# Kernel tuning notes

Hardware: AMD Instinct MI355X
Metric: run time of the kernel (lower is better)

## Reference

```python
import jax, jax.numpy as jnp
import numpy as np
from jax import lax

H = 512   # hidden_size
R = 4     # read heads
W = 32    # memory word size
N = 64    # memory cells
B = 64    # batch
T = 256   # seq len
IFACE = R * W + 3 * W + 5 * R + 3      # 247
HID_C = H + IFACE                       # 759 controller LSTM hidden
IN_C = H + R * W                        # 640 controller LSTM input
EPS = 1e-6


def setup_inputs() -> dict:
    key = jax.random.key(0)
    ks = jax.random.split(key, 7)
    s = 0.05
    return {
        "x": jax.random.normal(ks[0], (B, T, H), jnp.float32),
        "Wih_e": jax.random.normal(ks[1], (4 * H, H), jnp.float32) * s,
        "Whh_e": jax.random.normal(ks[2], (4 * H, H), jnp.float32) * s,
        "b_e": jnp.zeros((4 * H,), jnp.float32),
        "Wih_c": jax.random.normal(ks[3], (4 * HID_C, IN_C), jnp.float32) * s,
        "Whh_c": jax.random.normal(ks[4], (4 * HID_C, HID_C), jnp.float32) * s,
        "b_c": jnp.zeros((4 * HID_C,), jnp.float32),
    }


def lstm_cell(xt, h, c, Wih, Whh, b):
    g = xt @ Wih.T + h @ Whh.T + b
    i, f, gg, o = jnp.split(g, 4, axis=-1)  # PyTorch gate order i,f,g,o
    c = jax.nn.sigmoid(f) * c + jax.nn.sigmoid(i) * jnp.tanh(gg)
    h = jax.nn.sigmoid(o) * jnp.tanh(c)
    return h, c


def content_weights(M, keys, strengths):
    # M: [B,N,W], keys: [B,K,W], strengths: [B,K] -> softmaxed similarity [B,K,N]
    Mn = M * lax.rsqrt(jnp.sum(M * M, -1, keepdims=True) + EPS)
    kn = keys * lax.rsqrt(jnp.sum(keys * keys, -1, keepdims=True) + EPS)
    sim = jnp.einsum('bkw,bnw->bkn', kn, Mn)
    return jax.nn.softmax(sim * strengths[..., None], axis=-1)


def reference(x, Wih_e, Whh_e, b_e, Wih_c, Whh_c, b_c):
    # ---- encoder LSTM over time ----
    def enc_step(carry, xt):
        h, c = carry
        h, c = lstm_cell(xt, h, c, Wih_e, Whh_e, b_e)
        return (h, c), h

    z = jnp.zeros((B, H), x.dtype)
    _, enc = lax.scan(enc_step, (z, z), x.transpose(1, 0, 2))  # [T,B,H]

    # ---- controller LSTM + DNC memory per timestep ----
    eye = jnp.eye(N, dtype=x.dtype)

    def dnc_step(carry, e_t):
        h, c, M, u, p, L, wr, ww, rv = carry
        x_t = jnp.concatenate([e_t, rv], axis=-1)          # [B, H + R*W]
        h, c = lstm_cell(x_t, h, c, Wih_c, Whh_c, b_c)
        out = h[:, :H]
        xi = h[:, H:]                                       # [B, IFACE]
        o = 0
        read_keys = jnp.tanh(xi[:, :R * W].reshape(B, R, W)); o = R * W
        read_str = jax.nn.softplus(xi[:, o:o + R]); o += R
        write_key = jnp.tanh(xi[:, o:o + W]).reshape(B, 1, W); o += W
        write_str = jax.nn.softplus(xi[:, o:o + 1]); o += 1
        erase = jax.nn.sigmoid(xi[:, o:o + W]); o += W
        write_vec = jnp.tanh(xi[:, o:o + W]); o += W
        free_g = jax.nn.sigmoid(xi[:, o:o + R]); o += R
        alloc_g = jax.nn.sigmoid(xi[:, o:o + 1]); o += 1
        write_g = jax.nn.sigmoid(xi[:, o:o + 1]); o += 1
        read_modes = jax.nn.softmax(xi[:, o:o + 3 * R].reshape(B, R, 3), -1)
        # usage + retention
        psi = jnp.prod(1.0 - free_g[..., None] * wr, axis=1)   # [B,N]
        u = (u + ww - u * ww) * psi
        # allocation weighting via sorted usage
        idx = jnp.argsort(u, axis=-1)
        su = jnp.take_along_axis(u, idx, -1)
        cp = jnp.concatenate([jnp.ones((B, 1), u.dtype), jnp.cumprod(su, -1)[:, :-1]], -1)
        a = jnp.take_along_axis((1.0 - su) * cp, jnp.argsort(idx, -1), -1)
        # write weighting
        cw = content_weights(M, write_key, write_str)[:, 0]    # [B,N]
        ww = write_g * (alloc_g * a + (1.0 - alloc_g) * cw)
        # memory write
        M = M * (1.0 - ww[..., None] * erase[:, None, :]) + ww[..., None] * write_vec[:, None, :]
        # temporal link + precedence
        L = (1.0 - ww[:, :, None] - ww[:, None, :]) * L + ww[:, :, None] * p[:, None, :]
        L = L * (1.0 - eye)
        p = (1.0 - jnp.sum(ww, -1, keepdims=True)) * p + ww
        # read weighting: backward, content, forward modes
        cr = content_weights(M, read_keys, read_str)           # [B,R,N]
        fw = jnp.einsum('bnm,brm->brn', L, wr)
        bw = jnp.einsum('bmn,brm->brn', L, wr)
        wr = read_modes[..., 0:1] * bw + read_modes[..., 1:2] * cr + read_modes[..., 2:3] * fw
        rv = jnp.einsum('brn,bnw->brw', wr, M).reshape(B, R * W)
        return (h, c, M, u, p, L, wr, ww, rv), out

    init = (
        jnp.zeros((B, HID_C), x.dtype), jnp.zeros((B, HID_C), x.dtype),
        jnp.zeros((B, N, W), x.dtype), jnp.zeros((B, N), x.dtype),
        jnp.zeros((B, N), x.dtype), jnp.zeros((B, N, N), x.dtype),
        jnp.zeros((B, R, N), x.dtype), jnp.zeros((B, N), x.dtype),
        jnp.zeros((B, R * W), x.dtype),
    )
    _, outs = lax.scan(dnc_step, init, enc)   # [T,B,H]
    return outs.transpose(1, 0, 2)            # dnc_encoded [B,T,H]
```

## Files before the change

### kernel.cpp

```cpp
#include <hip/hip_runtime.h>
#include <math.h>


#define EPSF 1e-6f

__device__ __forceinline__ float sigmoidf_(float x) { return 1.f / (1.f + expf(-x)); }
__device__ __forceinline__ float softplusf_(float x) {
    return (x > 0.f) ? x + log1pf(expf(-x)) : log1pf(expf(x));
}
__device__ __forceinline__ void stg_coh(float* p, float v) {
    __hip_atomic_store(p, v, __ATOMIC_RELAXED, __HIP_MEMORY_SCOPE_AGENT);
}
__device__ __forceinline__ void st_flag(int* p, int v) {
    __hip_atomic_store(p, v, __ATOMIC_RELAXED, __HIP_MEMORY_SCOPE_AGENT);
}
__device__ __forceinline__ int ld_flag(const int* p) {
    return __hip_atomic_load(p, __ATOMIC_RELAXED, __HIP_MEMORY_SCOPE_AGENT);
}
__device__ __forceinline__ void poll256(const int* f, int lane, int tgt) {
    const int* p = f + lane * 32;
    for (;;) {
        int a = ld_flag(p);
        int b = ld_flag(p + 64 * 32);
        int c = ld_flag(p + 128 * 32);
        int d = ld_flag(p + 192 * 32);
        if (__all(min(min(a, b), min(c, d)) >= tgt)) break;
        __builtin_amdgcn_s_sleep(2);
    }
}
__device__ __forceinline__ void pollg(const int* f, int lane, int tgt) {
    const int* p = f + (64 + lane) * 32;
    for (;;) {
        int a = ld_flag(p);
        int b = ld_flag(p + 64 * 32);
        int c = ld_flag(p + 128 * 32);
        if (__all(min(min(a, b), c) >= tgt)) break;
        __builtin_amdgcn_s_sleep(2);
    }
}
__device__ __forceinline__ void pollx(const int* f, int lane, int tgt) {
    const int* p = f + (192 + (lane < 62 ? lane : 61)) * 32;
    while (!__all(ld_flag(p) >= tgt)) __builtin_amdgcn_s_sleep(2);
}
__device__ __forceinline__ void pollm(const int* f2, int lane, int tgt) {
    while (!__all(ld_flag(f2 + lane * 32) >= tgt)) __builtin_amdgcn_s_sleep(2);
}

__global__ __launch_bounds__(256) void prep_weights(const float* __restrict__ Whh_c,
                                                    const float* __restrict__ Wih_c,
                                                    float* __restrict__ Wcat) {
    int idx = blockIdx.x * 256 + threadIdx.x;
    if (idx < 3036 * 896) {
        int r = idx / 896, j = idx - r * 896;
        float v;
        if (j < 759) v = Whh_c[r * 759 + j];
        else if (j < 768) v = 0.f;
        else v = Wih_c[r * 640 + 512 + (j - 768)];
        Wcat[idx] = v;
    }
}

__global__ __launch_bounds__(256, 2) void proj_gemm(const float* __restrict__ A,
                                                    const float* __restrict__ W,
                                                    const float* __restrict__ bias,
                                                    float* __restrict__ OUT, int Ncols,
                                                    int wstride, int arow_base, int arow_stride_t,
                                                    int arow_stride_b, int arowlen, int Mrows) {
    __shared__ float As[16 * 68];
    __shared__ float Ws[16 * 68];
    const int tid = threadIdx.x;
    const int ntile = blockIdx.x, mtile = blockIdx.y;
    const int tx = tid & 15, ty = tid >> 4;
    const int lr = tid >> 2;
    const int lk = (tid & 3) * 4;
    const size_t arow =
        (size_t)arow_base + (size_t)mtile * arow_stride_t + (size_t)lr * arow_stride_b;
    const float* aptr = A + arow * arowlen + lk;
    const int wn = ntile * 64 + lr;
    const bool wok = (wn < Ncols);
    const float* wptr = W + (size_t)(wok ? wn : 0) * wstride + lk;
    float acc[4][4] = {};
    for (int kt = 0; kt < 512; kt += 16) {
        float4 av = *(const float4*)(aptr + kt);
        float4 w4l = *(const float4*)(wptr + kt);
        if (!wok) w4l = make_float4(0.f, 0.f, 0.f, 0.f);
        __syncthreads();
        As[(lk + 0) * 68 + lr] = av.x;
        As[(lk + 1) * 68 + lr] = av.y;
        As[(lk + 2) * 68 + lr] = av.z;
        As[(lk + 3) * 68 + lr] = av.w;
        Ws[(lk + 0) * 68 + lr] = w4l.x;
        Ws[(lk + 1) * 68 + lr] = w4l.y;
        Ws[(lk + 2) * 68 + lr] = w4l.z;
        Ws[(lk + 3) * 68 + lr] = w4l.w;
        __syncthreads();
#pragma unroll
        for (int k = 0; k < 16; ++k) {
            float4 a4 = *(const float4*)&As[k * 68 + ty * 4];
            float4 w4 = *(const float4*)&Ws[k * 68 + tx * 4];
            acc[0][0] = fmaf(a4.x, w4.x, acc[0][0]);
            acc[0][1] = fmaf(a4.x, w4.y, acc[0][1]);
            acc[0][2] = fmaf(a4.x, w4.z, acc[0][2]);
            acc[0][3] = fmaf(a4.x, w4.w, acc[0][3]);
            acc[1][0] = fmaf(a4.y, w4.x, acc[1][0]);
            acc[1][1] = fmaf(a4.y, w4.y, acc[1][1]);
            acc[1][2] = fmaf(a4.y, w4.z, acc[1][2]);
            acc[1][3] = fmaf(a4.y, w4.w, acc[1][3]);
            acc[2][0] = fmaf(a4.z, w4.x, acc[2][0]);
            acc[2][1] = fmaf(a4.z, w4.y, acc[2][1]);
            acc[2][2] = fmaf(a4.z, w4.z, acc[2][2]);
            acc[2][3] = fmaf(a4.z, w4.w, acc[2][3]);
            acc[3][0] = fmaf(a4.w, w4.x, acc[3][0]);
            acc[3][1] = fmaf(a4.w, w4.y, acc[3][1]);
            acc[3][2] = fmaf(a4.w, w4.z, acc[3][2]);
            acc[3][3] = fmaf(a4.w, w4.w, acc[3][3]);
        }
    }
    const int col0 = ntile * 64 + tx * 4;
    const int row0 = mtile * 64 + ty * 4;
#pragma unroll
    for (int j = 0; j < 4; ++j) {
        int col = col0 + j;
        if (col < Ncols) {
            float bv = bias[col];
            float4 st = make_float4(acc[0][j] + bv, acc[1][j] + bv, acc[2][j] + bv,
                                    acc[3][j] + bv);
            *(float4*)&OUT[(size_t)col * Mrows + row0] = st;
        }
    }
}

__global__ __launch_bounds__(256) void enc_emit(const float* __restrict__ HSE,
                                                float* __restrict__ ENC, int t0) {
    const int tl = blockIdx.x, bgrp = blockIdx.y;
    const int c4 = threadIdx.x & 127, b = bgrp * 2 + (threadIdx.x >> 7);
    float4 v = *(const float4*)&HSE[(size_t)tl * 32768 + c4 * 256 + b * 4];
    *(float4*)&ENC[((size_t)(t0 + tl) * 64 + b) * 512 + c4 * 4] = v;
}
__global__ __launch_bounds__(256) void out_emit(const float* __restrict__ HS,
                                                float* __restrict__ OUT, int t0) {
    const int tl = blockIdx.x, bgrp = blockIdx.y;
    const int c4 = threadIdx.x & 127, b = bgrp * 2 + (threadIdx.x >> 7);
    float4 v = *(const float4*)&HS[(size_t)tl * 57344 + c4 * 256 + b * 4];
    *(float4*)&OUT[(size_t)b * 131072 + (size_t)(t0 + tl) * 512 + c4 * 4] = v;
}

__global__ __launch_bounds__(512, 1) void enc_seq(const float* __restrict__ Whh,
                                                  const float* __restrict__ XPT,
                                                  float* __restrict__ HSE,
                                                  float* __restrict__ CE, int M, int TC,
                                                  int* flags) {
    __shared__ float part[8 * 4 * 64];
    const int tid = threadIdx.x;
    const int bk = blockIdx.x;
    const int lane = tid & 63;
    const int wv = __builtin_amdgcn_readfirstlane(tid >> 6);
    const int q = wv & 3, cidx = wv >> 2;
    const int cell = bk + 256 * cidx;
    const float* __restrict__ w0 = Whh + ((size_t)(0 * 512 + cell)) * 512 + q * 128;
    const float* __restrict__ w1 = Whh + ((size_t)(1 * 512 + cell)) * 512 + q * 128;
    const float* __restrict__ w2 = Whh + ((size_t)(2 * 512 + cell)) * 512 + q * 128;
    const float* __restrict__ w3 = Whh + ((size_t)(3 * 512 + cell)) * 512 + q * 128;
    float c_reg = 0.f;
    if (q == 0) c_reg = CE[cell * 64 + lane];
    for (int tl = 0; tl < TC; ++tl) {
        const float* rslot = HSE + (size_t)((tl + TC - 1) % TC) * 32768;
        float* wslot = HSE + (size_t)tl * 32768;
        float x0 = 0.f, x1 = 0.f, x2 = 0.f, x3 = 0.f;
        if (q == 0) {
            const int m = tl * 64 + lane;
            x0 = XPT[(size_t)(0 * 512 + cell) * M + m];
            x1 = XPT[(size_t)(1 * 512 + cell) * M + m];
            x2 = XPT[(size_t)(2 * 512 + cell) * M + m];
            x3 = XPT[(size_t)(3 * 512 + cell) * M + m];
        }
        float a0 = 0.f, a1 = 0.f, a2 = 0.f, a3 = 0.f;
        {
            const float4* __restrict__ hx = (const float4*)rslot + q * 32 * 64;
#pragma unroll 8
            for (int i = 0; i < 32; ++i) {
                float4 hv = hx[i * 64 + lane];
                float4 q0 = *(const float4*)&w0[i * 4];
                float4 q1 = *(const float4*)&w1[i * 4];
                float4 q2 = *(const float4*)&w2[i * 4];
                float4 q3 = *(const float4*)&w3[i * 4];
                a0 = fmaf(hv.x, q0.x, a0); a0 = fmaf(hv.y, q0.y, a0);
                a0 = fmaf(hv.z, q0.z, a0); a0 = fmaf(hv.w, q0.w, a0);
                a1 = fmaf(hv.x, q1.x, a1); a1 = fmaf(hv.y, q1.y, a1);
                a1 = fmaf(hv.z, q1.z, a1); a1 = fmaf(hv.w, q1.w, a1);
                a2 = fmaf(hv.x, q2.x, a2); a2 = fmaf(hv.y, q2.y, a2);
                a2 = fmaf(hv.z, q2.z, a2); a2 = fmaf(hv.w, q2.w, a2);
                a3 = fmaf(hv.x, q3.x, a3); a3 = fmaf(hv.y, q3.y, a3);
                a3 = fmaf(hv.z, q3.z, a3); a3 = fmaf(hv.w, q3.w, a3);
            }
        }
        part[(wv * 4 + 0) * 64 + lane] = a0;
        part[(wv * 4 + 1) * 64 + lane] = a1;
        part[(wv * 4 + 2) * 64 + lane] = a2;
        part[(wv * 4 + 3) * 64 + lane] = a3;
        __syncthreads();
        if (q == 0) {
            float g4[4];
#pragma unroll
            for (int g = 0; g < 4; ++g) {
                g4[g] = part[((cidx * 4 + 0) * 4 + g) * 64 + lane] +
                        part[((cidx * 4 + 1) * 4 + g) * 64 + lane] +
                        part[((cidx * 4 + 2) * 4 + g) * 64 + lane] +
                        part[((cidx * 4 + 3) * 4 + g) * 64 + lane];
            }
            float cc = sigmoidf_(g4[1] + x1) * c_reg + sigmoidf_(g4[0] + x0) * tanhf(g4[2] + x2);
            float hh = sigmoidf_(g4[3] + x3) * tanhf(cc);
            c_reg = cc;
            stg_coh(&wslot[(cell >> 2) * 256 + lane * 4 + (cell & 3)], hh);
        }
        __syncthreads();
        if (tid == 0) st_flag(flags + bk * 32, tl + 1);
        if (tl + 1 < TC) {
            if (wv == 0) poll256(flags, lane, tl + 1);
            __syncthreads();
        }
    }
    if (q == 0) CE[cell * 64 + lane] = c_reg;
}

__global__ __launch_bounds__(1024, 1) void dnc_seq(
    const float* __restrict__ Wcat, const float* __restrict__ CPT, float* __restrict__ HS,
    float* __restrict__ CC, float* __restrict__ Mg, float* __restrict__ Ug,
    float* __restrict__ Pg, float* __restrict__ WWg, float* __restrict__ Lg,
    float* __restrict__ WRg, int M, int TC, int* flags) {
    __shared__ float part[16 * 4 * 64];
    __shared__ float M_l[64 * 33];
    __shared__ float L_l[64 * 65];
    __shared__ float act[256];
    __shared__ float wr_l[256];
    __shared__ float u_l[64], p_l[64], ww_l[64], sM2[64], srt_l[64], asrt_l[64];
    __shared__ float modes_l[12], kss_l[4], scal[4];

    const int tid = threadIdx.x;
    const int bk = blockIdx.x;
    const int lane = tid & 63;
    const int wv = __builtin_amdgcn_readfirstlane(tid >> 6);
    const int q = wv & 3, cidx = wv >> 2;
    const bool machb = (bk < 64);
    const int cell_raw = machb ? 0 : (bk - 64) * 4 + cidx;
    const bool valid = !machb && (cell_raw < 759);
    const int cell = valid ? cell_raw : 0;
    const int b = bk;
    int* flags2 = flags + 8192;

    const float* __restrict__ wh0 = Wcat + (size_t)(0 * 759 + cell) * 896 + q * 192;
    const float* __restrict__ wh1 = Wcat + (size_t)(1 * 759 + cell) * 896 + q * 192;
    const float* __restrict__ wh2 = Wcat + (size_t)(2 * 759 + cell) * 896 + q * 192;
    const float* __restrict__ wh3 = Wcat + (size_t)(3 * 759 + cell) * 896 + q * 192;
    const float* __restrict__ wr0 = Wcat + (size_t)(0 * 759 + cell) * 896 + 768 + q * 32;
    const float* __restrict__ wr1 = Wcat + (size_t)(1 * 759 + cell) * 896 + 768 + q * 32;
    const float* __restrict__ wr2 = Wcat + (size_t)(2 * 759 + cell) * 896 + 768 + q * 32;
    const float* __restrict__ wr3 = Wcat + (size_t)(3 * 759 + cell) * 896 + 768 + q * 32;

    float c_reg = 0.f;
    if (valid && q == 0) c_reg = CC[cell * 64 + lane];

    if (machb) {
        if (tid < 256) {
#pragma unroll
            for (int i = 0; i < 8; ++i) {
                int e = tid + 256 * i;
                M_l[(e >> 5) * 33 + (e & 31)] = Mg[b * 2048 + e];
            }
#pragma unroll
            for (int i = 0; i < 16; ++i) {
                int e = tid + 256 * i;
                L_l[(e >> 6) * 65 + (e & 63)] = Lg[b * 4096 + e];
            }
            wr_l[tid] = WRg[b * 256 + tid];
        }
        if (tid < 64) {
            u_l[tid] = Ug[b * 64 + tid];
            p_l[tid] = Pg[b * 64 + tid];
            ww_l[tid] = WWg[b * 64 + tid];
        }
        __syncthreads();
    }

    float cp0 = 0.f, cp1 = 0.f, cp2 = 0.f, cp3 = 0.f;
    if (valid && q == 0) {
        cp0 = CPT[(size_t)(0 * 759 + cell) * M + lane];
        cp1 = CPT[(size_t)(1 * 759 + cell) * M + lane];
        cp2 = CPT[(size_t)(2 * 759 + cell) * M + lane];
        cp3 = CPT[(size_t)(3 * 759 + cell) * M + lane];
    }
    float A0 = 0.f, A1 = 0.f, A2 = 0.f, A3 = 0.f;
    if (valid) {
        const float4* __restrict__ hx = (const float4*)(HS + (size_t)(TC - 1) * 57344) + q * 48 * 64;
#pragma unroll 8
        for (int i = 0; i < 48; ++i) {
            float4 hv = hx[i * 64 + lane];
            float4 u0 = *(const float4*)&wh0[i * 4];
            float4 u1 = *(const float4*)&wh1[i * 4];
            float4 u2 = *(const float4*)&wh2[i * 4];
            float4 u3 = *(const float4*)&wh3[i * 4];
            A0 = fmaf(hv.x, u0.x, A0); A0 = fmaf(hv.y, u0.y, A0);
            A0 = fmaf(hv.z, u0.z, A0); A0 = fmaf(hv.w, u0.w, A0);
            A1 = fmaf(hv.x, u1.x, A1); A1 = fmaf(hv.y, u1.y, A1);
            A1 = fmaf(hv.z, u1.z, A1); A1 = fmaf(hv.w, u1.w, A1);
            A2 = fmaf(hv.x, u2.x, A2); A2 = fmaf(hv.y, u2.y, A2);
            A2 = fmaf(hv.z, u2.z, A2); A2 = fmaf(hv.w, u2.w, A2);
            A3 = fmaf(hv.x, u3.x, A3); A3 = fmaf(hv.y, u3.y, A3);
            A3 = fmaf(hv.z, u3.z, A3); A3 = fmaf(hv.w, u3.w, A3);
        }
    }

    for (int tl = 0; tl < TC; ++tl) {
        const bool last = (tl + 1 == TC);
        const float* rslot = HS + (size_t)((tl + TC - 1) % TC) * 57344;
        float* wslot = HS + (size_t)tl * 57344;
        if (!machb) {
            float b0 = 0.f, b1 = 0.f, b2 = 0.f, b3 = 0.f;
            if (valid) {
                const float4* __restrict__ hx = (const float4*)rslot + (192 + q * 8) * 64;
#pragma unroll
                for (int i = 0; i < 8; ++i) {
                    float4 hv = hx[i * 64 + lane];
                    float4 u0 = *(const float4*)&wr0[i * 4];
                    float4 u1 = *(const float4*)&wr1[i * 4];
                    float4 u2 = *(const float4*)&wr2[i * 4];
                    float4 u3 = *(const float4*)&wr3[i * 4];
                    b0 = fmaf(hv.x, u0.x, b0); b0 = fmaf(hv.y, u0.y, b0);
                    b0 = fmaf(hv.z, u0.z, b0); b0 = fmaf(hv.w, u0.w, b0);
                    b1 = fmaf(hv.x, u1.x, b1); b1 = fmaf(hv.y, u1.y, b1);
                    b1 = fmaf(hv.z, u1.z, b1); b1 = fmaf(hv.w, u1.w, b1);
                    b2 = fmaf(hv.x, u2.x, b2); b2 = fmaf(hv.y, u2.y, b2);
                    b2 = fmaf(hv.z, u2.z, b2); b2 = fmaf(hv.w, u2.w, b2);
                    b3 = fmaf(hv.x, u3.x, b3); b3 = fmaf(hv.y, u3.y, b3);
                    b3 = fmaf(hv.z, u3.z, b3); b3 = fmaf(hv.w, u3.w, b3);
                }
            }
            part[(wv * 4 + 0) * 64 + lane] = A0 + b0;
            part[(wv * 4 + 1) * 64 + lane] = A1 + b1;
            part[(wv * 4 + 2) * 64 + lane] = A2 + b2;
            part[(wv * 4 + 3) * 64 + lane] = A3 + b3;
            __syncthreads();
            if (valid && q == 0) {
                float g4[4];
#pragma unroll
                for (int g = 0; g < 4; ++g) {
                    g4[g] = part[((cidx * 4 + 0) * 4 + g) * 64 + lane] +
                            part[((cidx * 4 + 1) * 4 + g) * 64 + lane] +
                            part[((cidx * 4 + 2) * 4 + g) * 64 + lane] +
                            part[((cidx * 4 + 3) * 4 + g) * 64 + lane];
                }
                float cc =
                    sigmoidf_(g4[1] + cp1) * c_reg + sigmoidf_(g4[0] + cp0) * tanhf(g4[2] + cp2);
                float hh = sigmoidf_(g4[3] + cp3) * tanhf(cc);
                c_reg = cc;
                stg_coh(&wslot[(bk - 64) * 256 + lane * 4 + cidx], hh);
            }
            __syncthreads();
            if (tid == 0) st_flag(flags + bk * 32, tl + 1);
            if (!last) {
                if (wv == 0) pollg(flags, lane, tl + 1);
                __syncthreads();
                float np0 = 0.f, np1 = 0.f, np2 = 0.f, np3 = 0.f;
                if (valid && q == 0) {
                    const int m = (tl + 1) * 64 + lane;
                    np0 = CPT[(size_t)(0 * 759 + cell) * M + m];
                    np1 = CPT[(size_t)(1 * 759 + cell) * M + m];
                    np2 = CPT[(size_t)(2 * 759 + cell) * M + m];
                    np3 = CPT[(size_t)(3 * 759 + cell) * M + m];
                }
                A0 = A1 = A2 = A3 = 0.f;
                if (valid) {
                    const float4* __restrict__ hx = (const float4*)wslot + q * 48 * 64;
#pragma unroll 8
                    for (int i = 0; i < 48; ++i) {
                        float4 hv = hx[i * 64 + lane];
                        float4 u0 = *(const float4*)&wh0[i * 4];
                        float4 u1 = *(const float4*)&wh1[i * 4];
                        float4 u2 = *(const float4*)&wh2[i * 4];
                        float4 u3 = *(const float4*)&wh3[i * 4];
                        A0 = fmaf(hv.x, u0.x, A0); A0 = fmaf(hv.y, u0.y, A0);
                        A0 = fmaf(hv.z, u0.z, A0); A0 = fmaf(hv.w, u0.w, A0);
                        A1 = fmaf(hv.x, u1.x, A1); A1 = fmaf(hv.y, u1.y, A1);
                        A1 = fmaf(hv.z, u1.z, A1); A1 = fmaf(hv.w, u1.w, A1);
                        A2 = fmaf(hv.x, u2.x, A2); A2 = fmaf(hv.y, u2.y, A2);
                        A2 = fmaf(hv.z, u2.z, A2); A2 = fmaf(hv.w, u2.w, A2);
                        A3 = fmaf(hv.x, u3.x, A3); A3 = fmaf(hv.y, u3.y, A3);
                        A3 = fmaf(hv.z, u3.z, A3); A3 = fmaf(hv.w, u3.w, A3);
                    }
                }
                cp0 = np0; cp1 = np1; cp2 = np2; cp3 = np3;
                if (wv == 0) pollm(flags2, lane, tl + 1);
                __syncthreads();
            }
        } else {
            if (wv == 0) pollx(flags, lane, tl + 1);
            __syncthreads();
            if (tid < 247) {
                float v = wslot[(128 + (tid >> 2)) * 256 + b * 4 + (tid & 3)];
                float a;
                if (tid < 128) a = tanhf(v);
                else if (tid < 132) a = softplusf_(v);
                else if (tid < 164) a = tanhf(v);
                else if (tid == 164) a = softplusf_(v);
                else if (tid < 197) a = sigmoidf_(v);
                else if (tid < 229) a = tanhf(v);
                else if (tid < 235) a = sigmoidf_(v);
                else a = v;
                act[tid] = a;
            }
            if (tid < 64) {
                float s2 = 0.f;
                for (int w = 0; w < 32; ++w) {
                    float mm = M_l[tid * 33 + w];
                    s2 = fmaf(mm, mm, s2);
                }
                sM2[tid] = s2;
            }
            __syncthreads();
            if (tid < 64) {
                if (tid < 4) {
                    float m0 = act[235 + 3 * tid], m1 = act[236 + 3 * tid],
                          m2 = act[237 + 3 * tid];
                    float mx = fmaxf(m0, fmaxf(m1, m2));
                    float e0 = expf(m0 - mx), e1 = expf(m1 - mx), e2 = expf(m2 - mx);
                    float s = e0 + e1 + e2;
                    modes_l[3 * tid] = e0 / s;
                    modes_l[3 * tid + 1] = e1 / s;
                    modes_l[3 * tid + 2] = e2 / s;
                    float ks = 0.f;
                    for (int w = 0; w < 32; ++w) {
                        float kk = act[tid * 32 + w];
                        ks = fmaf(kk, kk, ks);
                    }
                    kss_l[tid] = ks;
                }
                if (tid == 4) {
                    float s = 0.f;
                    for (int w = 0; w < 32; ++w) {
                        float kk = act[132 + w];
                        s = fmaf(kk, kk, s);
                    }
                    scal[0] = s;
                }
                float psi = 1.f;
#pragma unroll
                for (int r = 0; r < 4; ++r) psi *= 1.f - act[229 + r] * wr_l[r * 64 + tid];
                float un = u_l[tid], wwo = ww_l[tid];
                float unew = (un + wwo - un * wwo) * psi;
                u_l[tid] = unew;
                int rk = 0;
                for (int m = 0; m < 64; ++m) {
                    float um = u_l[m];
                    rk += (um < unew) || (um == unew && m < tid);
                }
                srt_l[rk] = unew;
                float v = srt_l[tid];
                float incl = v;
#pragma unroll
                for (int off = 1; off < 64; off <<= 1) {
                    float o = __shfl_up(incl, off);
                    if (tid >= off) incl *= o;
                }
                float excl = __shfl_up(incl, 1);
                if (tid == 0) excl = 1.f;
                asrt_l[tid] = (1.f - v) * excl;
                float dot = 0.f;
                for (int w = 0; w < 32; ++w) dot = fmaf(act[132 + w], M_l[tid * 33 + w], dot);
                float logit = dot * rsqrtf(sM2[tid] + EPSF) * rsqrtf(scal[0] + EPSF) * act[164];
                float mx = logit;
#pragma unroll
                for (int off = 32; off; off >>= 1) mx = fmaxf(mx, __shfl_xor(mx, off));
                float e = expf(logit - mx);
                float s = e;
#pragma unroll
                for (int off = 32; off; off >>= 1) s += __shfl_xor(s, off);
                float cw = e / s;
                float a = asrt_l[rk];
                float agv = act[233], wgv = act[234];
                float wn = wgv * (agv * a + (1.f - agv) * cw);
                ww_l[tid] = wn;
                float sw = wn;
#pragma unroll
                for (int off = 32; off; off >>= 1) sw += __shfl_xor(sw, off);
                if (tid == 0) scal[1] = sw;
            }
            __syncthreads();
            if (tid < 256) {
#pragma unroll
                for (int i = 0; i < 8; ++i) {
                    int e = tid + 256 * i;
                    int n = e >> 5, w = e & 31;
                    float wwn = ww_l[n];
                    M_l[n * 33 + w] =
                        M_l[n * 33 + w] * (1.f - wwn * act[165 + w]) + wwn * act[197 + w];
                }
#pragma unroll
                for (int i = 0; i < 16; ++i) {
                    int e = tid + 256 * i;
                    int n = e >> 6, m = e & 63;
                    float Lv = L_l[n * 65 + m];
                    Lv = (1.f - ww_l[n] - ww_l[m]) * Lv + ww_l[n] * p_l[m];
                    L_l[n * 65 + m] = (n == m) ? 0.f : Lv;
                }
            }
            __syncthreads();
            float wrn = 0.f;
            if (tid < 256) {
                const int r = wv;
                const int n = lane;
                if (r == 0) p_l[n] = (1.f - scal[1]) * p_l[n] + ww_l[n];
                float s2 = 0.f;
                for (int w = 0; w < 32; ++w) {
                    float mm = M_l[n * 33 + w];
                    s2 = fmaf(mm, mm, s2);
                }
                float dot = 0.f;
                for (int w = 0; w < 32; ++w) dot = fmaf(act[r * 32 + w], M_l[n * 33 + w], dot);
                float logit = dot * rsqrtf(s2 + EPSF) * rsqrtf(kss_l[r] + EPSF) * act[128 + r];
                float mx = logit;
#pragma unroll
                for (int off = 32; off; off >>= 1) mx = fmaxf(mx, __shfl_xor(mx, off));
                float e = expf(logit - mx);
                float s = e;
#pragma unroll
                for (int off = 32; off; off >>= 1) s += __shfl_xor(s, off);
                float cr = e / s;
                float fw = 0.f, bw = 0.f;
                for (int m = 0; m < 64; ++m) {
                    float wrm = wr_l[r * 64 + m];
                    fw = fmaf(L_l[n * 65 + m], wrm, fw);
                    bw = fmaf(L_l[m * 65 + n], wrm, bw);
                }
                wrn = modes_l[r * 3] * bw + modes_l[r * 3 + 1] * cr + modes_l[r * 3 + 2] * fw;
            }
            __syncthreads();
            if (tid < 256) wr_l[tid] = wrn;
            __syncthreads();
            if (tid < 128) {
                const int r = tid >> 5, w = tid & 31;
                float rv = 0.f;
                for (int n = 0; n < 64; ++n) rv = fmaf(wr_l[r * 64 + n], M_l[n * 33 + w], rv);
                stg_coh(&wslot[(192 + (tid >> 2)) * 256 + b * 4 + (tid & 3)], rv);
            }
            __syncthreads();
            if (tid == 0) st_flag(flags2 + bk * 32, tl + 1);
        }
    }
    if (valid && q == 0) CC[cell * 64 + lane] = c_reg;
    if (machb) {
        if (tid < 256) {
#pragma unroll
            for (int i = 0; i < 8; ++i) {
                int e = tid + 256 * i;
                Mg[b * 2048 + e] = M_l[(e >> 5) * 33 + (e & 31)];
            }
#pragma unroll
            for (int i = 0; i < 16; ++i) {
                int e = tid + 256 * i;
                Lg[b * 4096 + e] = L_l[(e >> 6) * 65 + (e & 63)];
            }
            WRg[b * 256 + tid] = wr_l[tid];
        }
        if (tid < 64) {
            Ug[b * 64 + tid] = u_l[tid];
            Pg[b * 64 + tid] = p_l[tid];
            WWg[b * 64 + tid] = ww_l[tid];
        }
    }
}

extern "C" void kernel_launch(void* const* d_in, const int* in_sizes, int n_in, void* d_out,
                              int out_size, void* d_ws, size_t ws_size, hipStream_t stream) {
    const float* x = (const float*)d_in[0];
    const float* Wih_e = (const float*)d_in[1];
    const float* Whh_e = (const float*)d_in[2];
    const float* b_e = (const float*)d_in[3];
    const float* Wih_c = (const float*)d_in[4];
    const float* Whh_c = (const float*)d_in[5];
    const float* b_c = (const float*)d_in[6];
    float* out = (float*)d_out;
    float* ws = (float*)d_ws;

    int TC = 32;
    while (TC > 2) {
        size_t need =
            ((size_t)11612096 + (size_t)TC * 415488 + (size_t)(512 / TC) * 16384) * 4;
        if (need <= ws_size) break;
        TC >>= 1;
    }
    const int nch = 256 / TC;
    const int M = TC * 64;

    size_t off = 0;
    float* XPT = ws + off; off += (size_t)2048 * M;
    float* CPT = ws + off; off += (size_t)3036 * M;
    float* Wcat = ws + off; off += (size_t)3036 * 896;
    float* ENC = ws + off; off += (size_t)256 * 64 * 512;
    size_t zoff = off;
    float* HSE = ws + off; off += (size_t)TC * 32768;
    float* CE = ws + off; off += 512 * 64;
    float* HS = ws + off; off += (size_t)TC * 57344;
    float* CC = ws + off; off += 759 * 64;
    float* Mg = ws + off; off += 64 * 2048;
    float* Ug = ws + off; off += 64 * 64;
    float* Pg = ws + off; off += 64 * 64;
    float* WWg = ws + off; off += 64 * 64;
    float* Lg = ws + off; off += 64 * 4096;
    float* WRg = ws + off; off += 64 * 256;
    int* BAR = (int*)(ws + off); off += (size_t)2 * nch * 16384;
    size_t zbytes = (off - zoff) * 4;

    hipMemsetAsync(ws + zoff, 0, zbytes, stream);
    prep_weights<<<dim3((3036 * 896 + 255) / 256), dim3(256), 0, stream>>>(Whh_c, Wih_c, Wcat);
    for (int c = 0; c < nch; ++c) {
        proj_gemm<<<dim3(32, TC), dim3(256), 0, stream>>>(x, Wih_e, b_e, XPT, 2048, 512, c * TC,
                                                          1, 256, 512, M);
        enc_seq<<<dim3(256), dim3(512), 0, stream>>>(Whh_e, XPT, HSE, CE, M, TC,
                                                     BAR + (size_t)c * 16384);
        enc_emit<<<dim3(TC, 32), dim3(256), 0, stream>>>(HSE, ENC, c * TC);
    }
    for (int c = 0; c < nch; ++c) {
        proj_gemm<<<dim3(48, TC), dim3(256), 0, stream>>>(ENC, Wih_c, b_c, CPT, 3036, 640,
                                                          c * TC * 64, 64, 1, 512, M);
        dnc_seq<<<dim3(256), dim3(1024), 0, stream>>>(Wcat, CPT, HS, CC, Mg, Ug, Pg, WWg, Lg,
                                                      WRg, M, TC, BAR + (size_t)(nch + c) * 16384);
        out_emit<<<dim3(TC, 32), dim3(256), 0, stream>>>(HS, out, c * TC);
    }
}
```

Baseline: 8.132 ms.

## Repartition recurrent LSTM matvec so each wave covers 8 gate rows over narrower K

The encoder and controller recurrent matvecs are re-split so each wave accumulates 8 gate-cell rows (two cells × four gates) over a shorter K slice. This gives more reuse of each loaded hidden-state vector, and the final reduction sums 8 partials through shared memory. Flag arrays are packed contiguously instead of padded to 32-int strides, so a poll reads contiguous words in fewer cache lines, at the risk of false sharing on writes. The dnc_seq launch bound is raised to 4 waves per SIMD, which limits registers per thread and may cause spills.

After: 8.945 ms. +10.0%, slower.

```diff
diff --git a/kernel.cpp b/kernel.cpp
--- a/kernel.cpp
+++ b/kernel.cpp
@@ -18,32 +18,30 @@
     return __hip_atomic_load(p, __ATOMIC_RELAXED, __HIP_MEMORY_SCOPE_AGENT);
 }
 __device__ __forceinline__ void poll256(const int* f, int lane, int tgt) {
-    const int* p = f + lane * 32;
     for (;;) {
-        int a = ld_flag(p);
-        int b = ld_flag(p + 64 * 32);
-        int c = ld_flag(p + 128 * 32);
-        int d = ld_flag(p + 192 * 32);
+        int a = ld_flag(f + lane);
+        int b = ld_flag(f + 64 + lane);
+        int c = ld_flag(f + 128 + lane);
+        int d = ld_flag(f + 192 + lane);
         if (__all(min(min(a, b), min(c, d)) >= tgt)) break;
         __builtin_amdgcn_s_sleep(2);
     }
 }
 __device__ __forceinline__ void pollg(const int* f, int lane, int tgt) {
-    const int* p = f + (64 + lane) * 32;
     for (;;) {
-        int a = ld_flag(p);
-        int b = ld_flag(p + 64 * 32);
-        int c = ld_flag(p + 128 * 32);
+        int a = ld_flag(f + 64 + lane);
+        int b = ld_flag(f + 128 + lane);
+        int c = ld_flag(f + 192 + lane);
         if (__all(min(min(a, b), c) >= tgt)) break;
         __builtin_amdgcn_s_sleep(2);
     }
 }
 __device__ __forceinline__ void pollx(const int* f, int lane, int tgt) {
-    const int* p = f + (192 + (lane < 62 ? lane : 61)) * 32;
+    const int* p = f + 192 + (lane < 62 ? lane : 61);
     while (!__all(ld_flag(p) >= tgt)) __builtin_amdgcn_s_sleep(2);
 }
 __device__ __forceinline__ void pollm(const int* f2, int lane, int tgt) {
-    while (!__all(ld_flag(f2 + lane * 32) >= tgt)) __builtin_amdgcn_s_sleep(2);
+    while (!__all(ld_flag(f2 + lane) >= tgt)) __builtin_amdgcn_s_sleep(2);
 }
 
 __global__ __launch_bounds__(256) void prep_weights(const float* __restrict__ Whh_c,
@@ -150,85 +148,84 @@
                                                   float* __restrict__ HSE,
                                                   float* __restrict__ CE, int M, int TC,
                                                   int* flags) {
-    __shared__ float part[8 * 4 * 64];
+    __shared__ float part[8 * 8 * 64];
     const int tid = threadIdx.x;
     const int bk = blockIdx.x;
     const int lane = tid & 63;
     const int wv = __builtin_amdgcn_readfirstlane(tid >> 6);
-    const int q = wv & 3, cidx = wv >> 2;
-    const int cell = bk + 256 * cidx;
-    const float* __restrict__ w0 = Whh + ((size_t)(0 * 512 + cell)) * 512 + q * 128;
-    const float* __restrict__ w1 = Whh + ((size_t)(1 * 512 + cell)) * 512 + q * 128;
-    const float* __restrict__ w2 = Whh + ((size_t)(2 * 512 + cell)) * 512 + q * 128;
-    const float* __restrict__ w3 = Whh + ((size_t)(3 * 512 + cell)) * 512 + q * 128;
+    const int s = wv;
+
+    const float* wp[8];
+#pragma unroll
+    for (int cg = 0; cg < 8; ++cg) {
+        const int cell = (cg < 4) ? bk : bk + 256;
+        const int g = cg & 3;
+        wp[cg] = Whh + (size_t)(g * 512 + cell) * 512 + s * 64;
+    }
+    const bool gw = (wv < 2);
+    const int cellg = bk + 256 * (wv & 1);
     float c_reg = 0.f;
-    if (q == 0) c_reg = CE[cell * 64 + lane];
+    if (gw) c_reg = CE[cellg * 64 + lane];
+
     for (int tl = 0; tl < TC; ++tl) {
         const float* rslot = HSE + (size_t)((tl + TC - 1) % TC) * 32768;
         float* wslot = HSE + (size_t)tl * 32768;
-        float x0 = 0.f, x1 = 0.f, x2 = 0.f, x3 = 0.f;
-        if (q == 0) {
+        float x[4] = {};
+        if (gw) {
             const int m = tl * 64 + lane;
-            x0 = XPT[(size_t)(0 * 512 + cell) * M + m];
-            x1 = XPT[(size_t)(1 * 512 + cell) * M + m];
-            x2 = XPT[(size_t)(2 * 512 + cell) * M + m];
-            x3 = XPT[(size_t)(3 * 512 + cell) * M + m];
-        }
-        float a0 = 0.f, a1 = 0.f, a2 = 0.f, a3 = 0.f;
+#pragma unroll
+            for (int g = 0; g < 4; ++g) x[g] = XPT[(size_t)(g * 512 + cellg) * M + m];
+        }
+        float A[8] = {};
         {
-            const float4* __restrict__ hx = (const float4*)rslot + q * 32 * 64;
-#pragma unroll 8
-            for (int i = 0; i < 32; ++i) {
+            const float4* __restrict__ hx = (const float4*)rslot + s * 16 * 64;
+#pragma unroll 2
+            for (int i = 0; i < 16; ++i) {
                 float4 hv = hx[i * 64 + lane];
-                float4 q0 = *(const float4*)&w0[i * 4];
-                float4 q1 = *(const float4*)&w1[i * 4];
-                float4 q2 = *(const float4*)&w2[i * 4];
-                float4 q3 = *(const float4*)&w3[i * 4];
-                a0 = fmaf(hv.x, q0.x, a0); a0 = fmaf(hv.y, q0.y, a0);
-                a0 = fmaf(hv.z, q0.z, a0); a0 = fmaf(hv.w, q0.w, a0);
-                a1 = fmaf(hv.x, q1.x, a1); a1 = fmaf(hv.y, q1.y, a1);
-                a1 = fmaf(hv.z, q1.z, a1); a1 = fmaf(hv.w, q1.w, a1);
-                a2 = fmaf(hv.x, q2.x, a2); a2 = fmaf(hv.y, q2.y, a2);
-                a2 = fmaf(hv.z, q2.z, a2); a2 = fmaf(hv.w, q2.w, a2);
-                a3 = fmaf(hv.x, q3.x, a3); a3 = fmaf(hv.y, q3.y, a3);
-                a3 = fmaf(hv.z, q3.z, a3); a3 = fmaf(hv.w, q3.w, a3);
-            }
-        }
-        part[(wv * 4 + 0) * 64 + lane] = a0;
-        part[(wv * 4 + 1) * 64 + lane] = a1;
-        part[(wv * 4 + 2) * 64 + lane] = a2;
-        part[(wv * 4 + 3) * 64 + lane] = a3;
+#pragma unroll
+                for (int cg = 0; cg < 8; ++cg) {
+                    float4 w4 = *(const float4*)(wp[cg] + i * 4);
+                    A[cg] = fmaf(hv.x, w4.x, A[cg]);
+                    A[cg] = fmaf(hv.y, w4.y, A[cg]);
+                    A[cg] = fmaf(hv.z, w4.z, A[cg]);
+                    A[cg] = fmaf(hv.w, w4.w, A[cg]);
+                }
+            }
+        }
+#pragma unroll
+        for (int cg = 0; cg < 8; ++cg) part[(wv * 8 + cg) * 64 + lane] = A[cg];
         __syncthreads();
-        if (q == 0) {
+        if (gw) {
+            const int cl = wv & 1;
             float g4[4];
 #pragma unroll
             for (int g = 0; g < 4; ++g) {
-                g4[g] = part[((cidx * 4 + 0) * 4 + g) * 64 + lane] +
-                        part[((cidx * 4 + 1) * 4 + g) * 64 + lane] +
-                        part[((cidx * 4 + 2) * 4 + g) * 64 + lane] +
-                        part[((cidx * 4 + 3) * 4 + g) * 64 + lane];
-            }
-            float cc = sigmoidf_(g4[1] + x1) * c_reg + sigmoidf_(g4[0] + x0) * tanhf(g4[2] + x2);
-            float hh = sigmoidf_(g4[3] + x3) * tanhf(cc);
+                float sg = 0.f;
+#pragma unroll
+                for (int ss = 0; ss < 8; ++ss) sg += part[(ss * 8 + cl * 4 + g) * 64 + lane];
+                g4[g] = sg;
+            }
+            float cc = sigmoidf_(g4[1] + x[1]) * c_reg + sigmoidf_(g4[0] + x[0]) * tanhf(g4[2] + x[2]);
+            float hh = sigmoidf_(g4[3] + x[3]) * tanhf(cc);
             c_reg = cc;
-            stg_coh(&wslot[(cell >> 2) * 256 + lane * 4 + (cell & 3)], hh);
+            stg_coh(&wslot[(cellg >> 2) * 256 + lane * 4 + (cellg & 3)], hh);
         }
         __syncthreads();
-        if (tid == 0) st_flag(flags + bk * 32, tl + 1);
+        if (tid == 0) st_flag(flags + bk, tl + 1);
         if (tl + 1 < TC) {
             if (wv == 0) poll256(flags, lane, tl + 1);
             __syncthreads();
         }
     }
-    if (q == 0) CE[cell * 64 + lane] = c_reg;
-}
-
-__global__ __launch_bounds__(1024, 1) void dnc_seq(
+    if (gw) CE[cellg * 64 + lane] = c_reg;
+}
+
+__global__ __launch_bounds__(1024, 4) void dnc_seq(
     const float* __restrict__ Wcat, const float* __restrict__ CPT, float* __restrict__ HS,
     float* __restrict__ CC, float* __restrict__ Mg, float* __restrict__ Ug,
     float* __restrict__ Pg, float* __restrict__ WWg, float* __restrict__ Lg,
     float* __restrict__ WRg, int M, int TC, int* flags) {
-    __shared__ float part[16 * 4 * 64];
+    __shared__ float part[16 * 8 * 64];
     __shared__ float M_l[64 * 33];
     __shared__ float L_l[64 * 65];
     __shared__ float act[256];
@@ -240,25 +237,26 @@
     const int bk = blockIdx.x;
     const int lane = tid & 63;
     const int wv = __builtin_amdgcn_readfirstlane(tid >> 6);
-    const int q = wv & 3, cidx = wv >> 2;
+    const int s = wv & 7, p = wv >> 3;
     const bool machb = (bk < 64);
-    const int cell_raw = machb ? 0 : (bk - 64) * 4 + cidx;
-    const bool valid = !machb && (cell_raw < 759);
-    const int cell = valid ? cell_raw : 0;
+    const int base = machb ? 0 : (bk - 64) * 4;
     const int b = bk;
     int* flags2 = flags + 8192;
 
-    const float* __restrict__ wh0 = Wcat + (size_t)(0 * 759 + cell) * 896 + q * 192;
-    const float* __restrict__ wh1 = Wcat + (size_t)(1 * 759 + cell) * 896 + q * 192;
-    const float* __restrict__ wh2 = Wcat + (size_t)(2 * 759 + cell) * 896 + q * 192;
-    const float* __restrict__ wh3 = Wcat + (size_t)(3 * 759 + cell) * 896 + q * 192;
-    const float* __restrict__ wr0 = Wcat + (size_t)(0 * 759 + cell) * 896 + 768 + q * 32;
-    const float* __restrict__ wr1 = Wcat + (size_t)(1 * 759 + cell) * 896 + 768 + q * 32;
-    const float* __restrict__ wr2 = Wcat + (size_t)(2 * 759 + cell) * 896 + 768 + q * 32;
-    const float* __restrict__ wr3 = Wcat + (size_t)(3 * 759 + cell) * 896 + 768 + q * 32;
-
+    const float* wp[8];
+    const float* rp[8];
+#pragma unroll
+    for (int cg = 0; cg < 8; ++cg) {
+        int cell = base + p * 2 + (cg >> 2);
+        if (cell > 758) cell = 758;
+        const int g = cg & 3;
+        wp[cg] = Wcat + (size_t)(g * 759 + cell) * 896 + s * 96;
+        rp[cg] = Wcat + (size_t)(g * 759 + cell) * 896 + 768 + s * 16;
+    }
+    const int cellg = base + (wv & 3);
+    const bool gv = !machb && (wv < 4) && (cellg < 759);
     float c_reg = 0.f;
-    if (valid && q == 0) c_reg = CC[cell * 64 + lane];
+    if (gv) c_reg = CC[cellg * 64 + lane];
 
     if (machb) {
         if (tid < 256) {
@@ -282,113 +280,84 @@
         __syncthreads();
     }
 
-    float cp0 = 0.f, cp1 = 0.f, cp2 = 0.f, cp3 = 0.f;
-    if (valid && q == 0) {
-        cp0 = CPT[(size_t)(0 * 759 + cell) * M + lane];
-        cp1 = CPT[(size_t)(1 * 759 + cell) * M + lane];
-        cp2 = CPT[(size_t)(2 * 759 + cell) * M + lane];
-        cp3 = CPT[(size_t)(3 * 759 + cell) * M + lane];
-    }
-    float A0 = 0.f, A1 = 0.f, A2 = 0.f, A3 = 0.f;
-    if (valid) {
-        const float4* __restrict__ hx = (const float4*)(HS + (size_t)(TC - 1) * 57344) + q * 48 * 64;
-#pragma unroll 8
-        for (int i = 0; i < 48; ++i) {
-            float4 hv = hx[i * 64 + lane];
-            float4 u0 = *(const float4*)&wh0[i * 4];
-            float4 u1 = *(const float4*)&wh1[i * 4];
-            float4 u2 = *(const float4*)&wh2[i * 4];
-            float4 u3 = *(const float4*)&wh3[i * 4];
-            A0 = fmaf(hv.x, u0.x, A0); A0 = fmaf(hv.y, u0.y, A0);
-            A0 = fmaf(hv.z, u0.z, A0); A0 = fmaf(hv.w, u0.w, A0);
-            A1 = fmaf(hv.x, u1.x, A1); A1 = fmaf(hv.y, u1.y, A1);
-            A1 = fmaf(hv.z, u1.z, A1); A1 = fmaf(hv.w, u1.w, A1);
-            A2 = fmaf(hv.x, u2.x, A2); A2 = fmaf(hv.y, u2.y, A2);
-            A2 = fmaf(hv.z, u2.z, A2); A2 = fmaf(hv.w, u2.w, A2);
-            A3 = fmaf(hv.x, u3.x, A3); A3 = fmaf(hv.y, u3.y, A3);
-            A3 = fmaf(hv.z, u3.z, A3); A3 = fmaf(hv.w, u3.w, A3);
-        }
-    }
+#define ACC768(SLOT)                                                                 \
+    {                                                                                \
+        const float4* __restrict__ hx = (const float4*)(SLOT) + s * 24 * 64;         \
+        _Pragma("unroll 2") for (int i = 0; i < 24; ++i) {                           \
+            float4 hv = hx[i * 64 + lane];                                           \
+            _Pragma("unroll") for (int cg = 0; cg < 8; ++cg) {                       \
+                float4 w4 = *(const float4*)(wp[cg] + i * 4);                        \
+                A[cg] = fmaf(hv.x, w4.x, A[cg]);                                     \
+                A[cg] = fmaf(hv.y, w4.y, A[cg]);                                     \
+                A[cg] = fmaf(hv.z, w4.z, A[cg]);                                     \
+                A[cg] = fmaf(hv.w, w4.w, A[cg]);                                     \
+            }                                                                        \
+        }                                                                            \
+    }
+
+    float cp[4] = {};
+    if (gv) {
+#pragma unroll
+        for (int g = 0; g < 4; ++g) cp[g] = CPT[(size_t)(g * 759 + cellg) * M + lane];
+    }
+    float A[8] = {};
+    if (!machb) ACC768(HS + (size_t)(TC - 1) * 57344);
 
     for (int tl = 0; tl < TC; ++tl) {
         const bool last = (tl + 1 == TC);
         const float* rslot = HS + (size_t)((tl + TC - 1) % TC) * 57344;
         float* wslot = HS + (size_t)tl * 57344;
         if (!machb) {
-            float b0 = 0.f, b1 = 0.f, b2 = 0.f, b3 = 0.f;
-            if (valid) {
-                const float4* __restrict__ hx = (const float4*)rslot + (192 + q * 8) * 64;
-#pragma unroll
-                for (int i = 0; i < 8; ++i) {
+            {
+                const float4* __restrict__ hx = (const float4*)rslot + (192 + s * 4) * 64;
+#pragma unroll
+                for (int i = 0; i < 4; ++i) {
                     float4 hv = hx[i * 64 + lane];
-                    float4 u0 = *(const float4*)&wr0[i * 4];
-                    float4 u1 = *(const float4*)&wr1[i * 4];
-                    float4 u2 = *(const float4*)&wr2[i * 4];
-                    float4 u3 = *(const float4*)&wr3[i * 4];
-                    b0 = fmaf(hv.x, u0.x, b0); b0 = fmaf(hv.y, u0.y, b0);
-                    b0 = fmaf(hv.z, u0.z, b0); b0 = fmaf(hv.w, u0.w, b0);
-                    b1 = fmaf(hv.x, u1.x, b1); b1 = fmaf(hv.y, u1.y, b1);
-                    b1 = fmaf(hv.z, u1.z, b1); b1 = fmaf(hv.w, u1.w, b1);
-                    b2 = fmaf(hv.x, u2.x, b2); b2 = fmaf(hv.y, u2.y, b2);
-                    b2 = fmaf(hv.z, u2.z, b2); b2 = fmaf(hv.w, u2.w, b2);
-                    b3 = fmaf(hv.x, u3.x, b3); b3 = fmaf(hv.y, u3.y, b3);
-                    b3 = fmaf(hv.z, u3.z, b3); b3 = fmaf(hv.w, u3.w, b3);
-                }
-            }
-            part[(wv * 4 + 0) * 64 + lane] = A0 + b0;
-            part[(wv * 4 + 1) * 64 + lane] = A1 + b1;
-            part[(wv * 4 + 2) * 64 + lane] = A2 + b2;
-            part[(wv * 4 + 3) * 64 + lane] = A3 + b3;
-            __syncthreads();
-            if (valid && q == 0) {
+#pragma unroll
+                    for (int cg = 0; cg < 8; ++cg) {
+                        float4 w4 = *(const float4*)(rp[cg] + i * 4);
+                        A[cg] = fmaf(hv.x, w4.x, A[cg]);
+                        A[cg] = fmaf(hv.y, w4.y, A[cg]);
+                        A[cg] = fmaf(hv.z, w4.z, A[cg]);
+                        A[cg] = fmaf(hv.w, w4.w, A[cg]);
+                    }
+                }
+            }
+#pragma unroll
+            for (int cg = 0; cg < 8; ++cg) part[(wv * 8 + cg) * 64 + lane] = A[cg];
+            __syncthreads();
+            if (wv < 4) {
+                const int cl = wv & 1, pp = wv >> 1;
                 float g4[4];
 #pragma unroll
                 for (int g = 0; g < 4; ++g) {
-                    g4[g] = part[((cidx * 4 + 0) * 4 + g) * 64 + lane] +
-                            part[((cidx * 4 + 1) * 4 + g) * 64 + lane] +
-                            part[((cidx * 4 + 2) * 4 + g) * 64 + lane] +
-                            part[((cidx * 4 + 3) * 4 + g) * 64 + lane];
+                    float sg = 0.f;
+#pragma unroll
+                    for (int ss = 0; ss < 8; ++ss)
+                        sg += part[((pp * 8 + ss) * 8 + cl * 4 + g) * 64 + lane];
+                    g4[g] = sg;
                 }
                 float cc =
-                    sigmoidf_(g4[1] + cp1) * c_reg + sigmoidf_(g4[0] + cp0) * tanhf(g4[2] + cp2);
-                float hh = sigmoidf_(g4[3] + cp3) * tanhf(cc);
+                    sigmoidf_(g4[1] + cp[1]) * c_reg + sigmoidf_(g4[0] + cp[0]) * tanhf(g4[2] + cp[2]);
+                float hh = sigmoidf_(g4[3] + cp[3]) * tanhf(cc);
                 c_reg = cc;
-                stg_coh(&wslot[(bk - 64) * 256 + lane * 4 + cidx], hh);
-            }
-            __syncthreads();
-            if (tid == 0) st_flag(flags + bk * 32, tl + 1);
+                if (gv) stg_coh(&wslot[(bk - 64) * 256 + lane * 4 + wv], hh);
+            }
+            __syncthreads();
+            if (tid == 0) st_flag(flags + bk, tl + 1);
             if (!last) {
                 if (wv == 0) pollg(flags, lane, tl + 1);
                 __syncthreads();
-                float np0 = 0.f, np1 = 0.f, np2 = 0.f, np3 = 0.f;
-                if (valid && q == 0) {
+                float np[4] = {};
+                if (gv) {
                     const int m = (tl + 1) * 64 + lane;
-                    np0 = CPT[(size_t)(0 * 759 + cell) * M + m];
-                    np1 = CPT[(size_t)(1 * 759 + cell) * M + m];
-                    np2 = CPT[(size_t)(2 * 759 + cell) * M + m];
-                    np3 = CPT[(size_t)(3 * 759 + cell) * M + m];
-                }
-                A0 = A1 = A2 = A3 = 0.f;
-                if (valid) {
-                    const float4* __restrict__ hx = (const float4*)wslot + q * 48 * 64;
-#pragma unroll 8
-                    for (int i = 0; i < 48; ++i) {
-                        float4 hv = hx[i * 64 + lane];
-                        float4 u0 = *(const float4*)&wh0[i * 4];
-                        float4 u1 = *(const float4*)&wh1[i * 4];
-                        float4 u2 = *(const float4*)&wh2[i * 4];
-                        float4 u3 = *(const float4*)&wh3[i * 4];
-                        A0 = fmaf(hv.x, u0.x, A0); A0 = fmaf(hv.y, u0.y, A0);
-                        A0 = fmaf(hv.z, u0.z, A0); A0 = fmaf(hv.w, u0.w, A0);
-                        A1 = fmaf(hv.x, u1.x, A1); A1 = fmaf(hv.y, u1.y, A1);
-                        A1 = fmaf(hv.z, u1.z, A1); A1 = fmaf(hv.w, u1.w, A1);
-                        A2 = fmaf(hv.x, u2.x, A2); A2 = fmaf(hv.y, u2.y, A2);
-                        A2 = fmaf(hv.z, u2.z, A2); A2 = fmaf(hv.w, u2.w, A2);
-                        A3 = fmaf(hv.x, u3.x, A3); A3 = fmaf(hv.y, u3.y, A3);
-                        A3 = fmaf(hv.z, u3.z, A3); A3 = fmaf(hv.w, u3.w, A3);
-                    }
-                }
-                cp0 = np0; cp1 = np1; cp2 = np2; cp3 = np3;
+#pragma unroll
+                    for (int g = 0; g < 4; ++g) np[g] = CPT[(size_t)(g * 759 + cellg) * M + m];
+                }
+#pragma unroll
+                for (int cg = 0; cg < 8; ++cg) A[cg] = 0.f;
+                ACC768(wslot);
+                cp[0] = np[0]; cp[1] = np[1]; cp[2] = np[2]; cp[3] = np[3];
                 if (wv == 0) pollm(flags2, lane, tl + 1);
                 __syncthreads();
             }
@@ -423,10 +392,10 @@
                           m2 = act[237 + 3 * tid];
                     float mx = fmaxf(m0, fmaxf(m1, m2));
                     float e0 = expf(m0 - mx), e1 = expf(m1 - mx), e2 = expf(m2 - mx);
-                    float s = e0 + e1 + e2;
-                    modes_l[3 * tid] = e0 / s;
-                    modes_l[3 * tid + 1] = e1 / s;
-                    modes_l[3 * tid + 2] = e2 / s;
+                    float sm = e0 + e1 + e2;
+                    modes_l[3 * tid] = e0 / sm;
+                    modes_l[3 * tid + 1] = e1 / sm;
+                    modes_l[3 * tid + 2] = e2 / sm;
                     float ks = 0.f;
                     for (int w = 0; w < 32; ++w) {
                         float kk = act[tid * 32 + w];
@@ -435,12 +404,12 @@
                     kss_l[tid] = ks;
                 }
                 if (tid == 4) {
-                    float s = 0.f;
+                    float sm = 0.f;
                     for (int w = 0; w < 32; ++w) {
                         float kk = act[132 + w];
-                        s = fmaf(kk, kk, s);
+                        sm = fmaf(kk, kk, sm);
                     }
-                    scal[0] = s;
+                    scal[0] = sm;
                 }
                 float psi = 1.f;
 #pragma unroll
@@ -471,10 +440,10 @@
 #pragma unroll
                 for (int off = 32; off; off >>= 1) mx = fmaxf(mx, __shfl_xor(mx, off));
                 float e = expf(logit - mx);
-                float s = e;
-#pragma unroll
-                for (int off = 32; off; off >>= 1) s += __shfl_xor(s, off);
-                float cw = e / s;
+                float sm = e;
+#pragma unroll
+                for (int off = 32; off; off >>= 1) sm += __shfl_xor(sm, off);
+                float cw = e / sm;
                 float a = asrt_l[rk];
                 float agv = act[233], wgv = act[234];
                 float wn = wgv * (agv * a + (1.f - agv) * cw);
@@ -521,10 +490,10 @@
 #pragma unroll
                 for (int off = 32; off; off >>= 1) mx = fmaxf(mx, __shfl_xor(mx, off));
                 float e = expf(logit - mx);
-                float s = e;
-#pragma unroll
-                for (int off = 32; off; off >>= 1) s += __shfl_xor(s, off);
-                float cr = e / s;
+                float sm = e;
+#pragma unroll
+                for (int off = 32; off; off >>= 1) sm += __shfl_xor(sm, off);
+                float cr = e / sm;
                 float fw = 0.f, bw = 0.f;
                 for (int m = 0; m < 64; ++m) {
                     float wrm = wr_l[r * 64 + m];
@@ -543,10 +512,10 @@
                 stg_coh(&wslot[(192 + (tid >> 2)) * 256 + b * 4 + (tid & 3)], rv);
             }
             __syncthreads();
-            if (tid == 0) st_flag(flags2 + bk * 32, tl + 1);
-        }
-    }
-    if (valid && q == 0) CC[cell * 64 + lane] = c_reg;
+            if (tid == 0) st_flag(flags2 + bk, tl + 1);
+        }
+    }
+    if (gv) CC[cellg * 64 + lane] = c_reg;
     if (machb) {
         if (tid < 256) {
 #pragma unroll
```
